# Kernel optimization log

Measured on AMD Instinct MI355X. Metric: run time of the kernel, lower is better.

The kernel has to match this reference:

```python
import jax, jax.numpy as jnp
import numpy as np

NUM_HEADS = 4

def setup_inputs() -> dict:
    key = jax.random.key(0)
    ks = jax.random.split(key, 5)
    B, N, C = 2, 4096, 256
    s = 0.02
    return {
        "x": jax.random.normal(ks[0], (B, N, C), dtype=jnp.float32),
        "qkv_w": jax.random.normal(ks[1], (3 * C, C), dtype=jnp.float32) * s,
        "qkv_b": jax.random.normal(ks[2], (3 * C,), dtype=jnp.float32) * s,
        "out_w": jax.random.normal(ks[3], (C, C), dtype=jnp.float32) * s,
        "out_b": jax.random.normal(ks[4], (C,), dtype=jnp.float32) * s,
    }

def reference(x, qkv_w, qkv_b, out_w, out_b):
    # x: [B, N, C]; manual multi-head self-attention (eval mode, dropout off)
    B, N, C = x.shape
    H = NUM_HEADS
    D = C // H
    qkv = x @ qkv_w.T + qkv_b                      # [B, N, 3C]
    qkv = qkv.reshape(B, N, 3, H, D)
    qkv = jnp.transpose(qkv, (2, 0, 3, 1, 4))      # [3, B, H, N, D]
    q, k, v = qkv[0], qkv[1], qkv[2]
    scale = D ** -0.5
    attn = jnp.einsum('bhnd,bhmd->bhnm', q, k) * scale  # [B, H, N, N]
    attn = jax.nn.softmax(attn, axis=-1)
    out = jnp.einsum('bhnm,bhmd->bhnd', attn, v)   # [B, H, N, D]
    out = jnp.transpose(out, (0, 2, 1, 3)).reshape(B, N, C)
    return out @ out_w.T + out_b
```

## Files before the change

kernel.cpp:

```cpp
#include <hip/hip_runtime.h>

typedef __bf16 bf16x8 __attribute__((ext_vector_type(8)));
typedef float f32x4 __attribute__((ext_vector_type(4)));

#define MFMA_BF16(a, b, c) __builtin_amdgcn_mfma_f32_16x16x32_bf16((a), (b), (c), 0, 0, 0)

#define C1 0.18033688f

static __device__ __forceinline__ unsigned short f2bf(float f) {
    unsigned int u = __float_as_uint(f);
    unsigned int r = (u + 0x7fffu + ((u >> 16) & 1u)) >> 16;
    return (unsigned short)r;
}
static __device__ __forceinline__ float bf2f(unsigned short us) {
    return __uint_as_float(((unsigned int)us) << 16);
}
static __device__ __forceinline__ float exp2_hw(float x) {
    float r;
    asm("v_exp_f32 %0, %1" : "=v"(r) : "v"(x));
    return r;
}
static __device__ __forceinline__ unsigned pack_rh(float a, float b) {
    return __byte_perm(__float_as_uint(a) + 0x8000u, __float_as_uint(b) + 0x8000u, 0x7632);
}
static __device__ __forceinline__ void gload16(const void* g, void* l) {
    __builtin_amdgcn_global_load_lds(
        (const __attribute__((address_space(1))) unsigned int*)g,
        (__attribute__((address_space(3))) unsigned int*)l, 16, 0, 0);
}

static __device__ __forceinline__ void conv_seg(const void* src, unsigned short* dst, int n,
                                                int lb, bool f32) {
#pragma unroll
    for (int j = 0; j < 4; j++) {
        int idx = lb * 1024 + j * 256 + (int)threadIdx.x;
        if (idx < n) {
            dst[idx] = f32 ? f2bf(((const float*)src)[idx]) : ((const unsigned short*)src)[idx];
        }
    }
}

__global__ __launch_bounds__(256) void convert_kernel(
    const void* __restrict__ x, const void* __restrict__ qw, const void* __restrict__ qb,
    const void* __restrict__ ow, const void* __restrict__ ob,
    unsigned short* __restrict__ xb, unsigned short* __restrict__ qwb,
    unsigned short* __restrict__ qbb, unsigned short* __restrict__ owb,
    unsigned short* __restrict__ obb, int* __restrict__ flag) {
    __shared__ int tot;
    if (threadIdx.x == 0) tot = 0;
    __syncthreads();
    {
        unsigned short v = ((const unsigned short*)x)[threadIdx.x];
        int e = (v >> 7) & 0xFF;
        if (e >= 195) atomicAdd(&tot, 1);
    }
    __syncthreads();
    const bool f32 = (tot >= 8);
    if (blockIdx.x == 0 && threadIdx.x == 0) flag[0] = f32 ? 1 : 0;

    const int bid = blockIdx.x;
    if (bid < 2048)       conv_seg(x,  xb,  2097152, bid,        f32);
    else if (bid < 2240)  conv_seg(qw, qwb, 196608,  bid - 2048, f32);
    else if (bid < 2241)  conv_seg(qb, qbb, 768,     bid - 2240, f32);
    else if (bid < 2305)  conv_seg(ow, owb, 65536,   bid - 2241, f32);
    else                  conv_seg(ob, obb, 256,     bid - 2305, f32);
}

template <int BM, bool QKV>
__global__ __launch_bounds__(256) void gemm_kernel(
    const unsigned short* __restrict__ A, const unsigned short* __restrict__ W,
    const unsigned short* __restrict__ bias, unsigned short* __restrict__ Cb,
    float* __restrict__ Cf, const int* __restrict__ flag,
    unsigned short* __restrict__ Vt, int Nout) {
    constexpr int K = 256;
    constexpr int WPM = BM / 64;
    constexpr int IA = BM / 32;
    __shared__ __align__(16) char sm[BM * 128 + 8192];
    unsigned short* Alds = (unsigned short*)sm;
    unsigned short* Blds = (unsigned short*)(sm + BM * 128);

    const int tid = threadIdx.x;
    const int lane = tid & 63;
    const int wv = tid >> 6;
    const int m16 = lane & 15;
    const int quad = lane >> 4;
    const int bm = blockIdx.x * BM;
    const int bn = blockIdx.y * 64;

    int ago[IA];
    char* alp[IA];
#pragma unroll
    for (int i = 0; i < IA; i++) {
        const int c = wv * (BM * 2) + i * 64 + lane;
        const int r = c >> 3, g = (c & 7) ^ (r & 7);
        ago[i] = r * (K * 2) + g * 16;
        alp[i] = sm + c * 16;
    }
    int bgo[2];
    char* blp[2];
#pragma unroll
    for (int i = 0; i < 2; i++) {
        const int c = wv * 128 + i * 64 + lane;
        const int r = c >> 3, g = (c & 7) ^ (r & 7);
        bgo[i] = r * (K * 2) + g * 16;
        blp[i] = sm + BM * 128 + c * 16;
    }
    int aro[WPM][2], bro[4][2];
#pragma unroll
    for (int mb = 0; mb < WPM; mb++)
#pragma unroll
        for (int ks = 0; ks < 2; ks++) {
            const int row = wv * (WPM * 16) + mb * 16 + m16;
            aro[mb][ks] = row * 64 + ((4 * ks + quad) ^ (m16 & 7)) * 8;
        }
#pragma unroll
    for (int t = 0; t < 4; t++)
#pragma unroll
        for (int ks = 0; ks < 2; ks++) {
            const int row = t * 16 + m16;
            bro[t][ks] = row * 64 + ((4 * ks + quad) ^ (m16 & 7)) * 8;
        }

    const char* ag = (const char*)(A + (size_t)bm * K);
    const char* bg = (const char*)(W + (size_t)bn * K);

    f32x4 acc[WPM][4] = {};
#pragma unroll
    for (int kb = 0; kb < 4; kb++) {
        __syncthreads();
#pragma unroll
        for (int i = 0; i < IA; i++) gload16(ag + ago[i], alp[i]);
#pragma unroll
        for (int i = 0; i < 2; i++) gload16(bg + bgo[i], blp[i]);
        __syncthreads();
        ag += 128;
        bg += 128;
#pragma unroll
        for (int ks = 0; ks < 2; ks++) {
            bf16x8 bfr[4];
#pragma unroll
            for (int t = 0; t < 4; t++) bfr[t] = *(const bf16x8*)(Blds + bro[t][ks]);
#pragma unroll
            for (int mb = 0; mb < WPM; mb++) {
                const bf16x8 af = *(const bf16x8*)(Alds + aro[mb][ks]);
#pragma unroll
                for (int t = 0; t < 4; t++) acc[mb][t] = MFMA_BF16(af, bfr[t], acc[mb][t]);
            }
        }
    }

    const bool outf = (!QKV) && (flag != nullptr) && (*flag != 0);
#pragma unroll
    for (int mb = 0; mb < WPM; mb++) {
        const int row0 = bm + wv * (WPM * 16) + mb * 16 + quad * 4;
#pragma unroll
        for (int t = 0; t < 4; t++) {
            const int col = bn + t * 16 + m16;
            const float bv = bf2f(bias[col]);
            float v[4];
#pragma unroll
            for (int r = 0; r < 4; r++) v[r] = acc[mb][t][r] + bv;
            if (QKV) {
                if (col < 256) {
#pragma unroll
                    for (int r = 0; r < 4; r++)
                        Cb[(size_t)(row0 + r) * 768 + col] = f2bf(v[r] * C1);
                } else if (col < 512) {
#pragma unroll
                    for (int r = 0; r < 4; r++)
                        Cb[(size_t)(row0 + r) * 768 + col] = f2bf(v[r]);
                } else {
                    const int hh = (col - 512) >> 6, d = (col - 512) & 63;
                    const int bb = row0 >> 12, n0 = row0 & 4095;
                    uint2 w2;
                    w2.x = pack_rh(v[0], v[1]);
                    w2.y = pack_rh(v[2], v[3]);
                    *(uint2*)&Vt[((size_t)((bb * 4 + hh) * 64 + d)) * 4096 + n0] = w2;
                }
            } else {
                if (outf) {
#pragma unroll
                    for (int r = 0; r < 4; r++) Cf[(size_t)(row0 + r) * Nout + col] = v[r];
                } else {
#pragma unroll
                    for (int r = 0; r < 4; r++) Cb[(size_t)(row0 + r) * Nout + col] = f2bf(v[r]);
                }
            }
        }
    }
}

__global__ __launch_bounds__(256) void attn_kernel(
    const unsigned short* __restrict__ qkv, const unsigned short* __restrict__ Vt,
    unsigned short* __restrict__ attn, unsigned short* __restrict__ Opart,
    float* __restrict__ ml, int nsplit, int iters) {
    const int N = 4096, C3 = 768;
    __shared__ __align__(16) char sm[49152];
    unsigned short* Klds = (unsigned short*)sm;
    unsigned short* Vlds = (unsigned short*)(sm + 16384);
    unsigned short* Plds = (unsigned short*)(sm + 32768);

    const int tid = threadIdx.x;
    const int lane = tid & 63;
    const int wv = tid >> 6;
    const int m16 = lane & 15;
    const int quad = lane >> 4;

    const int qt = blockIdx.x & 63;
    const int bh = (blockIdx.x >> 6) & 7;
    const int kvs = blockIdx.x >> 9;
    const int b = bh >> 2, h = bh & 3;

    bf16x8 qf[4][2];
#pragma unroll
    for (int j = 0; j < 4; j++)
#pragma unroll
        for (int ks = 0; ks < 2; ks++)
            qf[j][ks] = *(const bf16x8*)(qkv + ((size_t)b * N + qt * 64 + j * 16 + m16) * C3 +
                                         h * 64 + ks * 32 + quad * 8);

    int kgo[4], vgo[4];
    char *klp[4], *vlp[4];
#pragma unroll
    for (int i = 0; i < 4; i++) {
        const int c = wv * 256 + i * 64 + lane;
        {
            const int r = c >> 3, g = (c & 7) ^ (r & 7);
            kgo[i] = r * 1536 + g * 16;
            klp[i] = sm + c * 16;
        }
        {
            const int d = c >> 4, g = (c & 15) ^ (d & 15);
            vgo[i] = d * 8192 + g * 16;
            vlp[i] = sm + 16384 + c * 16;
        }
    }
    int kro[2][2], vro[4], pwo[2][4], pro[4];
#pragma unroll
    for (int mb = 0; mb < 2; mb++)
#pragma unroll
        for (int ks = 0; ks < 2; ks++) {
            const int row = wv * 32 + mb * 16 + m16;
            kro[mb][ks] = row * 64 + ((4 * ks + quad) ^ (m16 & 7)) * 8;
        }
#pragma unroll
    for (int t = 0; t < 4; t++) vro[t] = (t * 16 + m16) * 128 + ((wv * 4 + quad) ^ m16) * 8;
#pragma unroll
    for (int mb = 0; mb < 2; mb++)
#pragma unroll
        for (int j = 0; j < 4; j++)
            pwo[mb][j] = wv * 2048 + (j * 16 + m16) * 32 +
                         ((2 * mb + (quad >> 1)) ^ (m16 & 3)) * 8 + (quad & 1) * 4;
#pragma unroll
    for (int j = 0; j < 4; j++)
        pro[j] = wv * 2048 + (j * 16 + m16) * 32 + (quad ^ (m16 & 3)) * 8;

    const char* kgp = (const char*)(qkv + (size_t)b * N * C3 + 256 + h * 64) +
                      (size_t)(kvs * iters) * 128 * 1536;
    const char* vgp = (const char*)(Vt + (size_t)bh * 64 * N) + (size_t)(kvs * iters) * 256;

    f32x4 o[4][4] = {};
    float lac[4] = {0.f, 0.f, 0.f, 0.f};

    for (int kt = 0; kt < iters; ++kt) {
        __syncthreads();
#pragma unroll
        for (int i = 0; i < 4; i++) {
            gload16(kgp + kgo[i], klp[i]);
            gload16(vgp + vgo[i], vlp[i]);
        }
        __syncthreads();
        kgp += 128 * 1536;
        vgp += 256;

        f32x4 s[2][4] = {};
#pragma unroll
        for (int mb = 0; mb < 2; mb++)
#pragma unroll
            for (int ks = 0; ks < 2; ks++) {
                const bf16x8 ka = *(const bf16x8*)(Klds + kro[mb][ks]);
#pragma unroll
                for (int j = 0; j < 4; j++) s[mb][j] = MFMA_BF16(ka, qf[j][ks], s[mb][j]);
            }

#pragma unroll
        for (int mb = 0; mb < 2; mb++)
#pragma unroll
            for (int j = 0; j < 4; j++) {
                const float p0 = exp2_hw(s[mb][j][0]);
                const float p1 = exp2_hw(s[mb][j][1]);
                const float p2 = exp2_hw(s[mb][j][2]);
                const float p3 = exp2_hw(s[mb][j][3]);
                lac[j] += (p0 + p1) + (p2 + p3);
                uint2 w;
                w.x = pack_rh(p0, p1);
                w.y = pack_rh(p2, p3);
                *(uint2*)(Plds + pwo[mb][j]) = w;
            }
        asm volatile("s_waitcnt lgkmcnt(0)" ::: "memory");

        bf16x8 pa[4];
#pragma unroll
        for (int j = 0; j < 4; j++) pa[j] = *(const bf16x8*)(Plds + pro[j]);
#pragma unroll
        for (int t = 0; t < 4; t++) {
            const bf16x8 vb = *(const bf16x8*)(Vlds + vro[t]);
#pragma unroll
            for (int j = 0; j < 4; j++) o[j][t] = MFMA_BF16(pa[j], vb, o[j][t]);
        }
    }

#pragma unroll
    for (int j = 0; j < 4; j++) {
        lac[j] += __shfl_xor(lac[j], 16);
        lac[j] += __shfl_xor(lac[j], 32);
    }
    __syncthreads();
    float* Ored = (float*)sm;
    float* lsum = (float*)(sm + 16384);
    if (quad == 0) {
#pragma unroll
        for (int j = 0; j < 4; j++) lsum[wv * 64 + j * 16 + m16] = lac[j];
    }
    const int row = tid >> 4;
    const int col = (tid & 15) * 4;
#pragma unroll
    for (int j = 0; j < 4; j++) {
#pragma unroll
        for (int t = 0; t < 4; t++)
#pragma unroll
            for (int r = 0; r < 4; r++)
                Ored[(wv * 16 + quad * 4 + r) * 64 + t * 16 + m16] = o[j][t][r];
        __syncthreads();
        f32x4 sum = *(f32x4*)&Ored[row * 64 + col];
        sum += *(f32x4*)&Ored[1024 + row * 64 + col];
        sum += *(f32x4*)&Ored[2048 + row * 64 + col];
        sum += *(f32x4*)&Ored[3072 + row * 64 + col];
        const float lq = lsum[j * 16 + row] + lsum[64 + j * 16 + row] +
                         lsum[128 + j * 16 + row] + lsum[192 + j * 16 + row];
        const int n = qt * 64 + j * 16 + row;
        if (nsplit == 1) {
            const float inv = 1.0f / lq;
            uint2 w;
            w.x = pack_rh(sum[0] * inv, sum[1] * inv);
            w.y = pack_rh(sum[2] * inv, sum[3] * inv);
            *(uint2*)&attn[((size_t)b * N + n) * 256 + h * 64 + col] = w;
        } else {
            uint2 w;
            w.x = pack_rh(sum[0], sum[1]);
            w.y = pack_rh(sum[2], sum[3]);
            *(uint2*)&Opart[(((size_t)(kvs * 8 + bh)) * N + n) * 64 + col] = w;
            if ((tid & 15) == 0) {
                float2 mv;
                mv.x = 0.0f;
                mv.y = lq;
                *(float2*)&ml[(((size_t)(kvs * 8 + bh)) * N + n) * 2] = mv;
            }
        }
        __syncthreads();
    }
}

__global__ __launch_bounds__(256) void merge_kernel(
    const unsigned short* __restrict__ Opart, const float* __restrict__ ml,
    unsigned short* __restrict__ attn, int nsplit) {
    const int N = 4096;
    const int gt = blockIdx.x * 256 + threadIdx.x;
    const int d = gt & 63;
    const int row = gt >> 6;
    const int bh = row >> 12;
    const int n = row & 4095;
    const int b = bh >> 2, h = bh & 3;

    float m = -INFINITY;
    for (int j = 0; j < nsplit; j++) m = fmaxf(m, ml[((size_t)(j * 8 + bh) * N + n) * 2]);
    float acc = 0.0f, l = 0.0f;
    for (int j = 0; j < nsplit; j++) {
        const size_t rbase = (size_t)(j * 8 + bh) * N + n;
        const float2 mv = *(const float2*)(&ml[rbase * 2]);
        const float w = exp2_hw(mv.x - m);
        l += w * mv.y;
        acc += w * bf2f(Opart[rbase * 64 + d]);
    }
    attn[((size_t)b * N + n) * 256 + h * 64 + d] = f2bf(acc / l);
}

extern "C" void kernel_launch(void* const* d_in, const int* in_sizes, int n_in,
                              void* d_out, int out_size, void* d_ws, size_t ws_size,
                              hipStream_t stream) {
    const int B = 2, N = 4096, H = 4;
    const int M = B * N;

    char* wsb = (char*)d_ws;
    int* flag = (int*)wsb;
    unsigned short* xb      = (unsigned short*)(wsb + 64);
    unsigned short* qwb     = xb + 2097152;
    unsigned short* qbb     = qwb + 196608;
    unsigned short* owb     = qbb + 768;
    unsigned short* obb     = owb + 65536;
    unsigned short* qkv_ws  = obb + 256;
    unsigned short* Vt_ws   = qkv_ws + 6291456;
    unsigned short* attn_ws = Vt_ws + 2097152;
    unsigned short* Opart   = attn_ws + 2097152;

    const size_t used = 64 + 2ull * (2097152 + 196608 + 768 + 65536 + 256 +
                                     6291456 + 2097152 + 2097152);
    const size_t perS = 8ull * 4096 * 64 * 2 + 8ull * 4096 * 2 * 4;
    int S = 1;
    if (ws_size >= used + 2 * perS + 128) S = 2;
    float* ml = (float*)(((uintptr_t)(Opart + (size_t)S * 2097152) + 15) & ~(uintptr_t)15);
    const int iters = N / (128 * S);

    convert_kernel<<<2306, 256, 0, stream>>>(d_in[0], d_in[1], d_in[2], d_in[3], d_in[4],
                                             xb, qwb, qbb, owb, obb, flag);

    gemm_kernel<128, true><<<dim3(M / 128, 768 / 64), 256, 0, stream>>>(
        xb, qwb, qbb, qkv_ws, nullptr, nullptr, Vt_ws, 768);

    attn_kernel<<<512 * S, 256, 0, stream>>>(qkv_ws, Vt_ws, attn_ws, Opart, ml, S, iters);

    if (S > 1) {
        merge_kernel<<<8 * N * 64 / 256, 256, 0, stream>>>(Opart, ml, attn_ws, S);
    }

    gemm_kernel<64, false><<<dim3(M / 64, 256 / 64), 256, 0, stream>>>(
        attn_ws, owb, obb, (unsigned short*)d_out, (float*)d_out, flag, nullptr, 256);
}
```

Before: 162.6 us.

## Register-prefetch next K/V and GEMM tiles instead of direct global-to-LDS loads

Replaces the global_load_lds direct-to-LDS copies in both the projection GEMM and the attention kernel with register staging: the next tile is loaded into registers while the current tile is computed, then written to LDS at the top of the next iteration. This overlaps global memory latency with MFMA work, at the cost of extra VGPRs and an extra LDS write pass. It also reorders the attention block index so heads vary fastest, changing which blocks run concurrently and share K/V in cache.

```diff
diff --git a/kernel.cpp b/kernel.cpp
--- a/kernel.cpp
+++ b/kernel.cpp
@@ -22,11 +22,6 @@
 }
 static __device__ __forceinline__ unsigned pack_rh(float a, float b) {
     return __byte_perm(__float_as_uint(a) + 0x8000u, __float_as_uint(b) + 0x8000u, 0x7632);
-}
-static __device__ __forceinline__ void gload16(const void* g, void* l) {
-    __builtin_amdgcn_global_load_lds(
-        (const __attribute__((address_space(1))) unsigned int*)g,
-        (__attribute__((address_space(3))) unsigned int*)l, 16, 0, 0);
 }
 
 static __device__ __forceinline__ void conv_seg(const void* src, unsigned short* dst, int n,
@@ -124,17 +119,29 @@
     const char* ag = (const char*)(A + (size_t)bm * K);
     const char* bg = (const char*)(W + (size_t)bn * K);
 
+    uint4 arg[IA], brg[2];
+#pragma unroll
+    for (int i = 0; i < IA; i++) arg[i] = *(const uint4*)(ag + ago[i]);
+#pragma unroll
+    for (int i = 0; i < 2; i++) brg[i] = *(const uint4*)(bg + bgo[i]);
+
     f32x4 acc[WPM][4] = {};
 #pragma unroll
     for (int kb = 0; kb < 4; kb++) {
         __syncthreads();
 #pragma unroll
-        for (int i = 0; i < IA; i++) gload16(ag + ago[i], alp[i]);
-#pragma unroll
-        for (int i = 0; i < 2; i++) gload16(bg + bgo[i], blp[i]);
+        for (int i = 0; i < IA; i++) *(uint4*)alp[i] = arg[i];
+#pragma unroll
+        for (int i = 0; i < 2; i++) *(uint4*)blp[i] = brg[i];
         __syncthreads();
         ag += 128;
         bg += 128;
+        if (kb < 3) {
+#pragma unroll
+            for (int i = 0; i < IA; i++) arg[i] = *(const uint4*)(ag + ago[i]);
+#pragma unroll
+            for (int i = 0; i < 2; i++) brg[i] = *(const uint4*)(bg + bgo[i]);
+        }
 #pragma unroll
         for (int ks = 0; ks < 2; ks++) {
             bf16x8 bfr[4];
@@ -206,8 +213,8 @@
     const int m16 = lane & 15;
     const int quad = lane >> 4;
 
-    const int qt = blockIdx.x & 63;
-    const int bh = (blockIdx.x >> 6) & 7;
+    const int bh = blockIdx.x & 7;
+    const int qt = (blockIdx.x >> 3) & 63;
     const int kvs = blockIdx.x >> 9;
     const int b = bh >> 2, h = bh & 3;
 
@@ -262,16 +269,30 @@
     f32x4 o[4][4] = {};
     float lac[4] = {0.f, 0.f, 0.f, 0.f};
 
+    uint4 kr[4], vr[4];
+#pragma unroll
+    for (int i = 0; i < 4; i++) {
+        kr[i] = *(const uint4*)(kgp + kgo[i]);
+        vr[i] = *(const uint4*)(vgp + vgo[i]);
+    }
+
     for (int kt = 0; kt < iters; ++kt) {
         __syncthreads();
 #pragma unroll
         for (int i = 0; i < 4; i++) {
-            gload16(kgp + kgo[i], klp[i]);
-            gload16(vgp + vgo[i], vlp[i]);
+            *(uint4*)klp[i] = kr[i];
+            *(uint4*)vlp[i] = vr[i];
         }
         __syncthreads();
         kgp += 128 * 1536;
         vgp += 256;
+        if (kt + 1 < iters) {
+#pragma unroll
+            for (int i = 0; i < 4; i++) {
+                kr[i] = *(const uint4*)(kgp + kgo[i]);
+                vr[i] = *(const uint4*)(vgp + vgo[i]);
+            }
+        }
 
         f32x4 s[2][4] = {};
 #pragma unroll
```

Result: slower. 290.5 us (+78.6%).

## Double-buffer LDS tiles in GEMM and attention, reorder attention block mapping

Applied to the files above, without the earlier changes.

Both the projection GEMM and the attention kernel now keep two LDS buffers. The next K/V (or A/W) tile is prefetched while the current one is computed, and the second barrier per iteration is removed. This is meant to hide global-load latency behind MFMA work. The attention kernel also writes P into the current K buffer to save LDS, and reorders blockIdx so batch-head varies fastest. LDS use grows, which can lower occupancy, and correctness depends on the async loads having completed before the single barrier.

```diff
diff --git a/kernel.cpp b/kernel.cpp
--- a/kernel.cpp
+++ b/kernel.cpp
@@ -75,9 +75,8 @@
     constexpr int K = 256;
     constexpr int WPM = BM / 64;
     constexpr int IA = BM / 32;
-    __shared__ __align__(16) char sm[BM * 128 + 8192];
-    unsigned short* Alds = (unsigned short*)sm;
-    unsigned short* Blds = (unsigned short*)(sm + BM * 128);
+    constexpr int ABYT = BM * 128;
+    __shared__ __align__(16) char sm[2 * ABYT + 16384];
 
     const int tid = threadIdx.x;
     const int lane = tid & 63;
@@ -87,23 +86,21 @@
     const int bm = blockIdx.x * BM;
     const int bn = blockIdx.y * 64;
 
-    int ago[IA];
-    char* alp[IA];
+    int ago[IA], alo[IA];
 #pragma unroll
     for (int i = 0; i < IA; i++) {
-        const int c = wv * (BM * 2) + i * 64 + lane;
+        const int c = wv * (IA * 64) + i * 64 + lane;
         const int r = c >> 3, g = (c & 7) ^ (r & 7);
         ago[i] = r * (K * 2) + g * 16;
-        alp[i] = sm + c * 16;
-    }
-    int bgo[2];
-    char* blp[2];
+        alo[i] = c * 16;
+    }
+    int bgo[2], blo[2];
 #pragma unroll
     for (int i = 0; i < 2; i++) {
         const int c = wv * 128 + i * 64 + lane;
         const int r = c >> 3, g = (c & 7) ^ (r & 7);
         bgo[i] = r * (K * 2) + g * 16;
-        blp[i] = sm + BM * 128 + c * 16;
+        blo[i] = c * 16;
     }
     int aro[WPM][2], bro[4][2];
 #pragma unroll
@@ -124,17 +121,28 @@
     const char* ag = (const char*)(A + (size_t)bm * K);
     const char* bg = (const char*)(W + (size_t)bn * K);
 
+#pragma unroll
+    for (int i = 0; i < IA; i++) gload16(ag + ago[i], sm + alo[i]);
+#pragma unroll
+    for (int i = 0; i < 2; i++) gload16(bg + bgo[i], sm + 2 * ABYT + blo[i]);
+
     f32x4 acc[WPM][4] = {};
 #pragma unroll
     for (int kb = 0; kb < 4; kb++) {
         __syncthreads();
-#pragma unroll
-        for (int i = 0; i < IA; i++) gload16(ag + ago[i], alp[i]);
-#pragma unroll
-        for (int i = 0; i < 2; i++) gload16(bg + bgo[i], blp[i]);
-        __syncthreads();
-        ag += 128;
-        bg += 128;
+        const int cur = kb & 1;
+        if (kb < 3) {
+            ag += 128;
+            bg += 128;
+            char* Adst = sm + (cur ^ 1) * ABYT;
+            char* Bdst = sm + 2 * ABYT + (cur ^ 1) * 8192;
+#pragma unroll
+            for (int i = 0; i < IA; i++) gload16(ag + ago[i], Adst + alo[i]);
+#pragma unroll
+            for (int i = 0; i < 2; i++) gload16(bg + bgo[i], Bdst + blo[i]);
+        }
+        const unsigned short* Alds = (const unsigned short*)(sm + cur * ABYT);
+        const unsigned short* Blds = (const unsigned short*)(sm + 2 * ABYT + cur * 8192);
 #pragma unroll
         for (int ks = 0; ks < 2; ks++) {
             bf16x8 bfr[4];
@@ -195,10 +203,7 @@
     unsigned short* __restrict__ attn, unsigned short* __restrict__ Opart,
     float* __restrict__ ml, int nsplit, int iters) {
     const int N = 4096, C3 = 768;
-    __shared__ __align__(16) char sm[49152];
-    unsigned short* Klds = (unsigned short*)sm;
-    unsigned short* Vlds = (unsigned short*)(sm + 16384);
-    unsigned short* Plds = (unsigned short*)(sm + 32768);
+    __shared__ __align__(16) char sm[65536];
 
     const int tid = threadIdx.x;
     const int lane = tid & 63;
@@ -206,8 +211,8 @@
     const int m16 = lane & 15;
     const int quad = lane >> 4;
 
-    const int qt = blockIdx.x & 63;
-    const int bh = (blockIdx.x >> 6) & 7;
+    const int bh = blockIdx.x & 7;
+    const int qt = (blockIdx.x >> 3) & 63;
     const int kvs = blockIdx.x >> 9;
     const int b = bh >> 2, h = bh & 3;
 
@@ -219,21 +224,16 @@
             qf[j][ks] = *(const bf16x8*)(qkv + ((size_t)b * N + qt * 64 + j * 16 + m16) * C3 +
                                          h * 64 + ks * 32 + quad * 8);
 
-    int kgo[4], vgo[4];
-    char *klp[4], *vlp[4];
+    int kgo[4], vgo[4], klo[4], vlo[4];
 #pragma unroll
     for (int i = 0; i < 4; i++) {
         const int c = wv * 256 + i * 64 + lane;
-        {
-            const int r = c >> 3, g = (c & 7) ^ (r & 7);
-            kgo[i] = r * 1536 + g * 16;
-            klp[i] = sm + c * 16;
-        }
-        {
-            const int d = c >> 4, g = (c & 15) ^ (d & 15);
-            vgo[i] = d * 8192 + g * 16;
-            vlp[i] = sm + 16384 + c * 16;
-        }
+        const int r = c >> 3, g = (c & 7) ^ (r & 7);
+        kgo[i] = r * 1536 + g * 16;
+        klo[i] = c * 16;
+        const int d = c >> 4, gg = (c & 15) ^ (d & 15);
+        vgo[i] = d * 8192 + gg * 16;
+        vlo[i] = c * 16;
     }
     int kro[2][2], vro[4], pwo[2][4], pro[4];
 #pragma unroll
@@ -259,26 +259,38 @@
                       (size_t)(kvs * iters) * 128 * 1536;
     const char* vgp = (const char*)(Vt + (size_t)bh * 64 * N) + (size_t)(kvs * iters) * 256;
 
+#pragma unroll
+    for (int i = 0; i < 4; i++) {
+        gload16(kgp + kgo[i], sm + klo[i]);
+        gload16(vgp + vgo[i], sm + 32768 + vlo[i]);
+    }
+
     f32x4 o[4][4] = {};
     float lac[4] = {0.f, 0.f, 0.f, 0.f};
 
     for (int kt = 0; kt < iters; ++kt) {
         __syncthreads();
-#pragma unroll
-        for (int i = 0; i < 4; i++) {
-            gload16(kgp + kgo[i], klp[i]);
-            gload16(vgp + vgo[i], vlp[i]);
-        }
-        __syncthreads();
-        kgp += 128 * 1536;
-        vgp += 256;
+        const int cur = kt & 1;
+        if (kt + 1 < iters) {
+            kgp += 128 * 1536;
+            vgp += 256;
+            char* Kdst = sm + (cur ^ 1) * 16384;
+            char* Vdst = sm + 32768 + (cur ^ 1) * 16384;
+#pragma unroll
+            for (int i = 0; i < 4; i++) {
+                gload16(kgp + kgo[i], Kdst + klo[i]);
+                gload16(vgp + vgo[i], Vdst + vlo[i]);
+            }
+        }
+        unsigned short* Kb = (unsigned short*)(sm + cur * 16384);
+        const unsigned short* Vb = (const unsigned short*)(sm + 32768 + cur * 16384);
 
         f32x4 s[2][4] = {};
 #pragma unroll
         for (int mb = 0; mb < 2; mb++)
 #pragma unroll
             for (int ks = 0; ks < 2; ks++) {
-                const bf16x8 ka = *(const bf16x8*)(Klds + kro[mb][ks]);
+                const bf16x8 ka = *(const bf16x8*)(Kb + kro[mb][ks]);
 #pragma unroll
                 for (int j = 0; j < 4; j++) s[mb][j] = MFMA_BF16(ka, qf[j][ks], s[mb][j]);
             }
@@ -295,16 +307,16 @@
                 uint2 w;
                 w.x = pack_rh(p0, p1);
                 w.y = pack_rh(p2, p3);
-                *(uint2*)(Plds + pwo[mb][j]) = w;
+                *(uint2*)(Kb + pwo[mb][j]) = w;
             }
         asm volatile("s_waitcnt lgkmcnt(0)" ::: "memory");
 
         bf16x8 pa[4];
 #pragma unroll
-        for (int j = 0; j < 4; j++) pa[j] = *(const bf16x8*)(Plds + pro[j]);
+        for (int j = 0; j < 4; j++) pa[j] = *(const bf16x8*)(Kb + pro[j]);
 #pragma unroll
         for (int t = 0; t < 4; t++) {
-            const bf16x8 vb = *(const bf16x8*)(Vlds + vro[t]);
+            const bf16x8 vb = *(const bf16x8*)(Vb + vro[t]);
 #pragma unroll
             for (int j = 0; j < 4; j++) o[j][t] = MFMA_BF16(pa[j], vb, o[j][t]);
         }
```

New measurement: 157.1 us. 3.4% less time.
